# Kernel optimization log

Hardware: AMD Instinct MI355X
Metric: run time of the kernel (lower is better)

## Reference

```python
import jax, jax.numpy as jnp
import numpy as np

IN_FEATURES = 4096
OUT_FEATURES = 11008
B, S = 4, 2048


def setup_inputs() -> dict:
    key = jax.random.key(0)
    k1, k2, k3, k4 = jax.random.split(key, 4)
    x = jax.random.normal(k1, (B, S, IN_FEATURES), dtype=jnp.float32)
    # packed uint8 bytes (two int4 nibbles per byte), stored as int32 in [0,256)
    qweight_packed = jax.random.randint(k2, (OUT_FEATURES, IN_FEATURES // 2), 0, 256, dtype=jnp.int32)
    # row-wise symmetric scales (positive, small)
    w_scales = jax.random.uniform(k3, (OUT_FEATURES, 1), dtype=jnp.float32) * 0.01 + 1e-4
    bias = jax.random.normal(k4, (OUT_FEATURES,), dtype=jnp.float32)
    return {"x": x, "qweight_packed": qweight_packed, "w_scales": w_scales, "bias": bias}


def _dequant(qweight_packed, w_scales, k_orig):
    # unpack two 4-bit nibbles per byte: low nibble first, then high nibble
    u = qweight_packed.astype(jnp.uint8)
    low = (u & 15).astype(jnp.int32)
    high = ((u >> 4) & 15).astype(jnp.int32)
    full = jnp.stack([low, high], axis=-1).reshape(u.shape[0], -1)[:, :k_orig]  # [N, K]
    w_int4 = jnp.where(full > 7, full - 16, full).astype(jnp.float32)
    return w_int4 * w_scales.astype(jnp.float32)  # [N, K]


def reference(x, qweight_packed, w_scales, bias):
    k = x.shape[-1]
    w = _dequant(qweight_packed, w_scales, k).astype(x.dtype)  # [N, K]
    x2 = x.reshape(-1, k)
    y2 = x2 @ w.T + bias.astype(x.dtype)
    return y2.reshape(*x.shape[:-1], w.shape[0])
```

## Files before the change

### kernel.cpp

```cpp
#include <hip/hip_runtime.h>
#include <stdint.h>

#define M_DIM 8192
#define N_DIM 11008
#define K_DIM 4096
#define KB_PACK 2048

#define BM 256
#define BN 256
#define BK 128
#define NKT (K_DIM / BK)
#define THREADS 512

typedef __attribute__((ext_vector_type(4))) int   i32x4;
typedef __attribute__((ext_vector_type(4))) float f32x4;

__device__ __forceinline__ void gload_lds16(const int8_t* g, int8_t* l) {
    __builtin_amdgcn_global_load_lds(
        (const __attribute__((address_space(1))) void*)g,
        (__attribute__((address_space(3))) void*)l,
        16, 0, 0);
}

__global__ __launch_bounds__(256) void quant_x_kernel(const float* __restrict__ x,
                                                      int8_t* __restrict__ xq,
                                                      float* __restrict__ xs) {
    const int m   = blockIdx.x;
    const int tid = threadIdx.x;
    const float4* row = (const float4*)(x + (size_t)m * K_DIM);

    float4 v[4];
    float amax = 0.f;
#pragma unroll
    for (int i = 0; i < 4; ++i) {
        v[i] = row[i * 256 + tid];
        amax = fmaxf(amax, fmaxf(fmaxf(fabsf(v[i].x), fabsf(v[i].y)),
                                 fmaxf(fabsf(v[i].z), fabsf(v[i].w))));
    }
#pragma unroll
    for (int off = 32; off > 0; off >>= 1)
        amax = fmaxf(amax, __shfl_xor(amax, off));
    __shared__ float red[4];
    if ((tid & 63) == 0) red[tid >> 6] = amax;
    __syncthreads();
    amax = fmaxf(fmaxf(red[0], red[1]), fmaxf(red[2], red[3]));

    const float safe = fmaxf(amax, 1e-20f);
    const float inv  = 127.f / safe;
    if (tid == 0) xs[m] = safe * (1.f / 127.f);

    int* out = (int*)(xq + (size_t)m * K_DIM);
#pragma unroll
    for (int i = 0; i < 4; ++i) {
        int c0 = __float2int_rn(v[i].x * inv);
        int c1 = __float2int_rn(v[i].y * inv);
        int c2 = __float2int_rn(v[i].z * inv);
        int c3 = __float2int_rn(v[i].w * inv);
        out[i * 256 + tid] = (c0 & 255) | ((c1 & 255) << 8) | ((c2 & 255) << 16) | (c3 << 24);
    }
}

__device__ __forceinline__ int unpack2(int v0, int v1) {
    int l0 = (((v0 & 15) ^ 8) - 8) & 255;
    int h0 = ((((v0 >> 4) & 15) ^ 8) - 8) & 255;
    int l1 = (((v1 & 15) ^ 8) - 8) & 255;
    int h1 = ((((v1 >> 4) & 15) ^ 8) - 8) & 255;
    return l0 | (h0 << 8) | (l1 << 16) | (h1 << 24);
}

__global__ __launch_bounds__(256) void unpack_w_kernel(const int* __restrict__ qw,
                                                       int8_t* __restrict__ wq) {
    size_t i = (size_t)blockIdx.x * 256 + threadIdx.x;
    const i32x4* q4 = (const i32x4*)qw;
    i32x4 a = q4[2 * i];
    i32x4 b = q4[2 * i + 1];
    i32x4 o;
    o.x = unpack2(a.x, a.y);
    o.y = unpack2(a.z, a.w);
    o.z = unpack2(b.x, b.y);
    o.w = unpack2(b.z, b.w);
    ((i32x4*)wq)[i] = o;
}

__global__ __launch_bounds__(THREADS, 2) void gemm_i8_kernel(
    const int8_t* __restrict__ A,
    const int8_t* __restrict__ B,
    const float* __restrict__ xs,
    const float* __restrict__ wsc,
    const float* __restrict__ bias,
    float* __restrict__ C) {
    __shared__ int8_t lds[131072];

    const int tid  = threadIdx.x;
    const int lane = tid & 63;
    const int wid  = tid >> 6;
    const int wr   = wid >> 2;
    const int wc   = wid & 3;
    const int l15  = lane & 15;
    const int q    = lane >> 4;

    const int lin = blockIdx.y * gridDim.x + blockIdx.x;
    const int swz = (lin & 7) * 172 + (lin >> 3);
    const int m0  = (swz & 31) * BM;
    const int n0  = (swz >> 5) * BN;

    const int sr   = tid >> 2;
    const int scol = (((tid & 3) ^ ((tid >> 3) & 3)) << 4);
    const int8_t* gA = A + (size_t)(m0 + sr) * K_DIM + scol;
    const int8_t* gB = B + (size_t)(n0 + sr) * K_DIM + scol;
    const int sdst = tid * 16;

#define STAGE_A(KT, S) do { \
        const int8_t* g_ = gA + (size_t)(KT) * BK + (S) * 64; \
        int8_t* d_ = lds + (((KT) & 1) << 15) + ((S) << 14) + sdst; \
        gload_lds16(g_, d_); \
        gload_lds16(g_ + (size_t)128 * K_DIM, d_ + 8192); \
    } while (0)
#define STAGE_B(KT, S) do { \
        const int8_t* g_ = gB + (size_t)(KT) * BK + (S) * 64; \
        int8_t* d_ = lds + 65536 + (((KT) & 1) << 15) + ((S) << 14) + sdst; \
        gload_lds16(g_, d_); \
        gload_lds16(g_ + (size_t)128 * K_DIM, d_ + 8192); \
    } while (0)

    const int fswz = ((q ^ ((l15 >> 1) & 3)) << 4);
    const int aoff = (wr * 128 + l15) * 64 + fswz;
    const int boff = 65536 + (wc * 64 + l15) * 64 + fswz;

#define LDA(MI, SS, BS) (*(const i32x4*)(lds + (aoff + (BS) + (SS) * 16384 + (MI) * 1024)))
#define LDB(NI, SS, BS) (*(const i32x4*)(lds + (boff + (BS) + (SS) * 16384 + (NI) * 1024)))
#define MFMA(D, AOP, BOP) D = __builtin_amdgcn_mfma_i32_16x16x64_i8(AOP, BOP, D, 0, 0, 0)

    i32x4 acc[8][4] = {};

    STAGE_A(0, 0); STAGE_B(0, 0); STAGE_A(0, 1); STAGE_B(0, 1);
    STAGE_A(1, 0); STAGE_B(1, 0); STAGE_A(1, 1);
    asm volatile("s_waitcnt vmcnt(6)" ::: "memory");
    __builtin_amdgcn_s_barrier();

    for (int kt = 0; kt < NKT; ++kt) {
        const int bsel = (kt & 1) << 15;
        const int s1 = (kt + 1 < NKT) ? kt + 1 : kt - 1;
        const int s2 = (kt + 2 < NKT) ? kt + 2 : kt;
        i32x4 af[8], bf0, bf1, bf2, bf3;

#pragma unroll
        for (int mi = 0; mi < 8; ++mi) af[mi] = LDA(mi, 0, bsel);
        bf0 = LDB(0, 0, bsel);
        bf1 = LDB(1, 0, bsel);
        STAGE_B(s1, 1);
        __builtin_amdgcn_s_barrier();
        __builtin_amdgcn_s_setprio(1);
#pragma unroll
        for (int mi = 0; mi < 8; ++mi) { MFMA(acc[mi][0], af[mi], bf0); MFMA(acc[mi][1], af[mi], bf1); }
        __builtin_amdgcn_s_setprio(0);
        __builtin_amdgcn_s_barrier();

        bf2 = LDB(2, 0, bsel);
        bf3 = LDB(3, 0, bsel);
        STAGE_A(s2, 0);
        __builtin_amdgcn_s_barrier();
        __builtin_amdgcn_s_setprio(1);
#pragma unroll
        for (int mi = 0; mi < 8; ++mi) { MFMA(acc[mi][2], af[mi], bf2); MFMA(acc[mi][3], af[mi], bf3); }
        __builtin_amdgcn_s_setprio(0);
        __builtin_amdgcn_s_barrier();

#pragma unroll
        for (int mi = 0; mi < 8; ++mi) af[mi] = LDA(mi, 1, bsel);
        bf0 = LDB(0, 1, bsel);
        bf1 = LDB(1, 1, bsel);
        STAGE_B(s2, 0);
        __builtin_amdgcn_s_barrier();
        __builtin_amdgcn_s_setprio(1);
#pragma unroll
        for (int mi = 0; mi < 8; ++mi) { MFMA(acc[mi][0], af[mi], bf0); MFMA(acc[mi][1], af[mi], bf1); }
        __builtin_amdgcn_s_setprio(0);
        __builtin_amdgcn_s_barrier();

        bf2 = LDB(2, 1, bsel);
        bf3 = LDB(3, 1, bsel);
        STAGE_A(s2, 1);
        __builtin_amdgcn_s_barrier();
        __builtin_amdgcn_s_setprio(1);
#pragma unroll
        for (int mi = 0; mi < 8; ++mi) { MFMA(acc[mi][2], af[mi], bf2); MFMA(acc[mi][3], af[mi], bf3); }
        __builtin_amdgcn_s_setprio(0);
        asm volatile("s_waitcnt vmcnt(6)" ::: "memory");
        __builtin_amdgcn_s_barrier();
    }

    const int row0 = q * 4;
    float sn[4], bv[4];
#pragma unroll
    for (int ni = 0; ni < 4; ++ni) {
        const int n = n0 + wc * 64 + ni * 16 + l15;
        sn[ni] = wsc[n];
        bv[ni] = bias[n];
    }
#pragma unroll
    for (int mi = 0; mi < 8; ++mi) {
        const int mbase = m0 + wr * 128 + mi * 16 + row0;
        float sm[4];
#pragma unroll
        for (int ri = 0; ri < 4; ++ri) sm[ri] = xs[mbase + ri];
#pragma unroll
        for (int ni = 0; ni < 4; ++ni) {
            const int n = n0 + wc * 64 + ni * 16 + l15;
            float* cp = C + (size_t)mbase * N_DIM + n;
#pragma unroll
            for (int ri = 0; ri < 4; ++ri)
                cp[(size_t)ri * N_DIM] = (float)acc[mi][ni][ri] * (sm[ri] * sn[ni]) + bv[ni];
        }
    }
#undef STAGE_A
#undef STAGE_B
#undef LDA
#undef LDB
#undef MFMA
}

__global__ void fallback_kernel(const float* __restrict__ x, const int* __restrict__ qw,
                                const float* __restrict__ sc, const float* __restrict__ bias,
                                float* __restrict__ y) {
    int m = blockIdx.y;
    int n = blockIdx.x * 256 + threadIdx.x;
    __shared__ float xsh[K_DIM];
    for (int k = threadIdx.x; k < K_DIM; k += 256) xsh[k] = x[(size_t)m * K_DIM + k];
    __syncthreads();
    if (n < N_DIM) {
        float acc = 0.f;
        const int* qr = qw + (size_t)n * KB_PACK;
        for (int kb = 0; kb < KB_PACK; ++kb) {
            int v = qr[kb] & 255;
            int lo = v & 15; lo -= (lo & 8) << 1;
            int hi = (v >> 4) & 15; hi -= (hi & 8) << 1;
            acc += xsh[2 * kb] * (float)lo + xsh[2 * kb + 1] * (float)hi;
        }
        y[(size_t)m * N_DIM + n] = acc * sc[n] + bias[n];
    }
}

extern "C" void kernel_launch(void* const* d_in, const int* in_sizes, int n_in,
                              void* d_out, int out_size, void* d_ws, size_t ws_size,
                              hipStream_t stream) {
    const float* x    = (const float*)d_in[0];
    const int*   qw   = (const int*)d_in[1];
    const float* sc   = (const float*)d_in[2];
    const float* bias = (const float*)d_in[3];
    float*       y    = (float*)d_out;

    const size_t xq_bytes = (size_t)M_DIM * K_DIM;
    const size_t wq_bytes = (size_t)N_DIM * K_DIM;
    const size_t xs_bytes = (size_t)M_DIM * sizeof(float);
    const size_t need = xq_bytes + wq_bytes + xs_bytes;

    if (ws_size >= need) {
        int8_t* xq = (int8_t*)d_ws;
        int8_t* wq = xq + xq_bytes;
        float*  xs = (float*)(wq + wq_bytes);
        quant_x_kernel<<<M_DIM, 256, 0, stream>>>(x, xq, xs);
        unpack_w_kernel<<<(int)((size_t)N_DIM * K_DIM / 16 / 256), 256, 0, stream>>>(qw, wq);
        gemm_i8_kernel<<<dim3(N_DIM / BN, M_DIM / BM), THREADS, 0, stream>>>(xq, wq, xs, sc, bias, y);
    } else {
        fallback_kernel<<<dim3((N_DIM + 255) / 256, M_DIM), 256, 0, stream>>>(x, qw, sc, bias, y);
    }
}
```

Baseline: 885.0 us.

## Switch int8 GEMM main loop to triple-buffered BK=64 pipeline with one barrier

Halves the K tile to 64 and replaces the double-buffered, four-phase loop (eight barriers per iteration) with a three-slot rotating LDS ring. Each iteration issues loads two tiles ahead, runs all 32 MFMAs, then waits and synchronises once. This cuts barrier overhead and shrinks LDS from 128KB to 96KB. In exchange there are twice as many loop iterations, so less MFMA work is done per synchronisation.

```diff
diff --git a/kernel.cpp b/kernel.cpp
--- a/kernel.cpp
+++ b/kernel.cpp
@@ -8,7 +8,7 @@
 
 #define BM 256
 #define BN 256
-#define BK 128
+#define BK 64
 #define NKT (K_DIM / BK)
 #define THREADS 512
 
@@ -89,7 +89,7 @@
     const float* __restrict__ wsc,
     const float* __restrict__ bias,
     float* __restrict__ C) {
-    __shared__ int8_t lds[131072];
+    __shared__ int8_t lds[98304];
 
     const int tid  = threadIdx.x;
     const int lane = tid & 63;
@@ -110,84 +110,66 @@
     const int8_t* gB = B + (size_t)(n0 + sr) * K_DIM + scol;
     const int sdst = tid * 16;
 
-#define STAGE_A(KT, S) do { \
-        const int8_t* g_ = gA + (size_t)(KT) * BK + (S) * 64; \
-        int8_t* d_ = lds + (((KT) & 1) << 15) + ((S) << 14) + sdst; \
+#define STAGE_A(GK, DB) do { \
+        const int8_t* g_ = gA + (size_t)(GK) * BK; \
+        int8_t* d_ = lds + (DB) + sdst; \
         gload_lds16(g_, d_); \
         gload_lds16(g_ + (size_t)128 * K_DIM, d_ + 8192); \
     } while (0)
-#define STAGE_B(KT, S) do { \
-        const int8_t* g_ = gB + (size_t)(KT) * BK + (S) * 64; \
-        int8_t* d_ = lds + 65536 + (((KT) & 1) << 15) + ((S) << 14) + sdst; \
+#define STAGE_B(GK, DB) do { \
+        const int8_t* g_ = gB + (size_t)(GK) * BK; \
+        int8_t* d_ = lds + (DB) + sdst; \
         gload_lds16(g_, d_); \
         gload_lds16(g_ + (size_t)128 * K_DIM, d_ + 8192); \
     } while (0)
 
     const int fswz = ((q ^ ((l15 >> 1) & 3)) << 4);
     const int aoff = (wr * 128 + l15) * 64 + fswz;
-    const int boff = 65536 + (wc * 64 + l15) * 64 + fswz;
-
-#define LDA(MI, SS, BS) (*(const i32x4*)(lds + (aoff + (BS) + (SS) * 16384 + (MI) * 1024)))
-#define LDB(NI, SS, BS) (*(const i32x4*)(lds + (boff + (BS) + (SS) * 16384 + (NI) * 1024)))
+    const int boff = (wc * 64 + l15) * 64 + fswz;
+
+#define LD(BASE, OFF) (*(const i32x4*)(lds + (BASE) + (OFF)))
 #define MFMA(D, AOP, BOP) D = __builtin_amdgcn_mfma_i32_16x16x64_i8(AOP, BOP, D, 0, 0, 0)
 
+    int aRd = 0,     aNx = 16384, aSt = 32768;
+    int bRd = 49152, bNx = 65536, bSt = 81920;
+
     i32x4 acc[8][4] = {};
 
-    STAGE_A(0, 0); STAGE_B(0, 0); STAGE_A(0, 1); STAGE_B(0, 1);
-    STAGE_A(1, 0); STAGE_B(1, 0); STAGE_A(1, 1);
-    asm volatile("s_waitcnt vmcnt(6)" ::: "memory");
+    STAGE_A(0, aRd); STAGE_B(0, bRd);
+    STAGE_A(1, aNx); STAGE_B(1, bNx);
+    asm volatile("s_waitcnt vmcnt(4)" ::: "memory");
     __builtin_amdgcn_s_barrier();
 
     for (int kt = 0; kt < NKT; ++kt) {
-        const int bsel = (kt & 1) << 15;
-        const int s1 = (kt + 1 < NKT) ? kt + 1 : kt - 1;
-        const int s2 = (kt + 2 < NKT) ? kt + 2 : kt;
-        i32x4 af[8], bf0, bf1, bf2, bf3;
-
-#pragma unroll
-        for (int mi = 0; mi < 8; ++mi) af[mi] = LDA(mi, 0, bsel);
-        bf0 = LDB(0, 0, bsel);
-        bf1 = LDB(1, 0, bsel);
-        STAGE_B(s1, 1);
+        const int gk = (kt + 2 < NKT) ? kt + 2 : 0;
+        STAGE_A(gk, aSt);
+        STAGE_B(gk, bSt);
+
+        i32x4 af[4], ag[4], bf[4];
+#pragma unroll
+        for (int i = 0; i < 4; ++i) af[i] = LD(aRd, aoff + i * 1024);
+#pragma unroll
+        for (int i = 0; i < 4; ++i) bf[i] = LD(bRd, boff + i * 1024);
+#pragma unroll
+        for (int i = 0; i < 4; ++i) ag[i] = LD(aRd, aoff + (4 + i) * 1024);
+
+        __builtin_amdgcn_s_setprio(1);
+#pragma unroll
+        for (int mi = 0; mi < 4; ++mi)
+#pragma unroll
+            for (int ni = 0; ni < 4; ++ni) MFMA(acc[mi][ni], af[mi], bf[ni]);
+#pragma unroll
+        for (int mi = 0; mi < 4; ++mi)
+#pragma unroll
+            for (int ni = 0; ni < 4; ++ni) MFMA(acc[4 + mi][ni], ag[mi], bf[ni]);
+        __builtin_amdgcn_s_setprio(0);
+
+        asm volatile("s_waitcnt vmcnt(4)" ::: "memory");
         __builtin_amdgcn_s_barrier();
-        __builtin_amdgcn_s_setprio(1);
-#pragma unroll
-        for (int mi = 0; mi < 8; ++mi) { MFMA(acc[mi][0], af[mi], bf0); MFMA(acc[mi][1], af[mi], bf1); }
-        __builtin_amdgcn_s_setprio(0);
-        __builtin_amdgcn_s_barrier();
-
-        bf2 = LDB(2, 0, bsel);
-        bf3 = LDB(3, 0, bsel);
-        STAGE_A(s2, 0);
-        __builtin_amdgcn_s_barrier();
-        __builtin_amdgcn_s_setprio(1);
-#pragma unroll
-        for (int mi = 0; mi < 8; ++mi) { MFMA(acc[mi][2], af[mi], bf2); MFMA(acc[mi][3], af[mi], bf3); }
-        __builtin_amdgcn_s_setprio(0);
-        __builtin_amdgcn_s_barrier();
-
-#pragma unroll
-        for (int mi = 0; mi < 8; ++mi) af[mi] = LDA(mi, 1, bsel);
-        bf0 = LDB(0, 1, bsel);
-        bf1 = LDB(1, 1, bsel);
-        STAGE_B(s2, 0);
-        __builtin_amdgcn_s_barrier();
-        __builtin_amdgcn_s_setprio(1);
-#pragma unroll
-        for (int mi = 0; mi < 8; ++mi) { MFMA(acc[mi][0], af[mi], bf0); MFMA(acc[mi][1], af[mi], bf1); }
-        __builtin_amdgcn_s_setprio(0);
-        __builtin_amdgcn_s_barrier();
-
-        bf2 = LDB(2, 1, bsel);
-        bf3 = LDB(3, 1, bsel);
-        STAGE_A(s2, 1);
-        __builtin_amdgcn_s_barrier();
-        __builtin_amdgcn_s_setprio(1);
-#pragma unroll
-        for (int mi = 0; mi < 8; ++mi) { MFMA(acc[mi][2], af[mi], bf2); MFMA(acc[mi][3], af[mi], bf3); }
-        __builtin_amdgcn_s_setprio(0);
-        asm volatile("s_waitcnt vmcnt(6)" ::: "memory");
-        __builtin_amdgcn_s_barrier();
+
+        int t;
+        t = aRd; aRd = aNx; aNx = aSt; aSt = t;
+        t = bRd; bRd = bNx; bNx = bSt; bSt = t;
     }
 
     const int row0 = q * 4;
@@ -215,8 +197,7 @@
     }
 #undef STAGE_A
 #undef STAGE_B
-#undef LDA
-#undef LDB
+#undef LD
 #undef MFMA
 }
 
```

After: 875.7 us. No clear change (-1.1%).
